# Optimization experiments

Measured on AMD Instinct MI355X. Metric: run time of the kernel, lower is better.

Reference implementation:

```python
import jax, jax.numpy as jnp
import numpy as np

H = 1024
V_IN = 32000
V_OUT = 32000
MAX_LEN = 512
SOS = 0


def _gru_cell(x, h, W_ih, W_hh, b_ih, b_hh):
    # PyTorch GRU cell: gates ordered (r, z, n)
    gi = W_ih @ x + b_ih            # [3H]
    gh = W_hh @ h + b_hh            # [3H]
    i_r, i_z, i_n = jnp.split(gi, 3)
    h_r, h_z, h_n = jnp.split(gh, 3)
    r = jax.nn.sigmoid(i_r + h_r)
    z = jax.nn.sigmoid(i_z + h_z)
    n = jnp.tanh(i_n + r * h_n)
    return (1.0 - z) * n + z * h


def setup_inputs() -> dict:
    key = jax.random.key(0)
    ks = jax.random.split(key, 20)
    s = 0.02
    f = jnp.float32
    d = {}
    d["input_tensor"] = jax.random.randint(ks[0], (512,), 0, V_IN)
    d["target_tensor"] = jax.random.randint(ks[1], (512,), 0, V_OUT)
    d["enc_emb"] = jax.random.normal(ks[2], (V_IN, H), f) * s
    d["enc_W_ih"] = jax.random.normal(ks[3], (3 * H, H), f) * s
    d["enc_W_hh"] = jax.random.normal(ks[4], (3 * H, H), f) * s
    d["enc_b_ih"] = jnp.zeros((3 * H,), f)
    d["enc_b_hh"] = jnp.zeros((3 * H,), f)
    d["dec_emb"] = jax.random.normal(ks[5], (V_OUT, H), f) * s
    d["attn_W"] = jax.random.normal(ks[6], (MAX_LEN, 2 * H), f) * s
    d["attn_b"] = jnp.zeros((MAX_LEN,), f)
    d["comb_W"] = jax.random.normal(ks[7], (H, 2 * H), f) * s
    d["comb_b"] = jnp.zeros((H,), f)
    d["dec_W_ih"] = jax.random.normal(ks[8], (3 * H, H), f) * s
    d["dec_W_hh"] = jax.random.normal(ks[9], (3 * H, H), f) * s
    d["dec_b_ih"] = jnp.zeros((3 * H,), f)
    d["dec_b_hh"] = jnp.zeros((3 * H,), f)
    d["out_W"] = jax.random.normal(ks[10], (V_OUT, H), f) * s
    d["out_b"] = jnp.zeros((V_OUT,), f)
    return d


def reference(input_tensor, target_tensor, enc_emb, enc_W_ih, enc_W_hh,
              enc_b_ih, enc_b_hh, dec_emb, attn_W, attn_b, comb_W, comb_b,
              dec_W_ih, dec_W_hh, dec_b_ih, dec_b_hh, out_W, out_b):
    # --- encoder: per-token GRU ---
    def enc_step(h, tok):
        x = enc_emb[tok]
        h2 = _gru_cell(x, h, enc_W_ih, enc_W_hh, enc_b_ih, enc_b_hh)
        return h2, h2

    h0 = jnp.zeros((H,), enc_emb.dtype)
    h_final, enc_outs = jax.lax.scan(enc_step, h0, input_tensor)
    # zero-padded encoder memory of size max_length (as in original)
    enc_full = jnp.zeros((MAX_LEN, H), enc_outs.dtype).at[: enc_outs.shape[0]].set(enc_outs)

    # --- decoder (teacher forcing): inputs are [SOS, target[:-1]] ---
    dec_in = jnp.concatenate([jnp.array([SOS], dtype=target_tensor.dtype),
                              target_tensor[:-1]])

    def dec_step(h, inp):
        tok, tgt = inp
        e = dec_emb[tok]                                        # [H]
        aw = jax.nn.softmax(attn_W @ jnp.concatenate([e, h]) + attn_b)  # [MAX_LEN]
        applied = aw @ enc_full                                 # [H]
        x = jax.nn.relu(comb_W @ jnp.concatenate([e, applied]) + comb_b)
        h2 = _gru_cell(x, h, dec_W_ih, dec_W_hh, dec_b_ih, dec_b_hh)
        logp = jax.nn.log_softmax(out_W @ h2 + out_b)           # [V_OUT]
        return h2, -logp[tgt]

    _, nll = jax.lax.scan(dec_step, h_final, (dec_in, target_tensor))
    return jnp.sum(nll) / target_tensor.shape[0]
```

## Files before the change

### kernel.cpp

```cpp
#include <hip/hip_runtime.h>
#include <math.h>


#define H 1024
#define T 512
#define V 32000

typedef unsigned long long u64;

__device__ __forceinline__ void st_agent_f32(float* p, float v) {
    __hip_atomic_store(p, v, __ATOMIC_RELAXED, __HIP_MEMORY_SCOPE_AGENT);
}
__device__ __forceinline__ float2 ld_agent_f2(const float* p) {
    u64 u = __hip_atomic_load((const u64*)p, __ATOMIC_RELAXED,
                              __HIP_MEMORY_SCOPE_AGENT);
    float2 t;
    __builtin_memcpy(&t, &u, 8);
    return t;
}
__device__ __forceinline__ void st_slot(unsigned* p, unsigned v) {
    __hip_atomic_store(p, v, __ATOMIC_RELAXED, __HIP_MEMORY_SCOPE_AGENT);
}
__device__ __forceinline__ unsigned ld_slot(const unsigned* p) {
    return __hip_atomic_load(p, __ATOMIC_RELAXED, __HIP_MEMORY_SCOPE_AGENT);
}

__device__ __forceinline__ void poll_slots(const unsigned* slots, unsigned val,
                                           int lane) {
    for (;;) {
        unsigned a = ld_slot(slots + (lane      ) * 16);
        unsigned b = ld_slot(slots + (lane +  64) * 16);
        unsigned c = ld_slot(slots + (lane + 128) * 16);
        unsigned d = ld_slot(slots + (lane + 192) * 16);
        int ok = (a >= val) & (b >= val) & (c >= val) & (d >= val);
        if (__all(ok)) break;
    }
}

__device__ __forceinline__ float sigmoidf_(float x) { return 1.f / (1.f + expf(-x)); }

__global__ __launch_bounds__(256) void gemm_tn(
    const float* __restrict__ X, int xs, int xo,
    const int* __restrict__ gidx, int gmode,
    const float* __restrict__ W, int wsd, int wo,
    const float* __restrict__ bias,
    float* __restrict__ C, int cs, int K)
{
    __shared__ float A_lds[32][64];
    __shared__ float B_lds[32][64];
    const int tid = threadIdx.x;
    const int tx = tid & 15, ty = tid >> 4;
    const int n0 = blockIdx.x * 64, t0 = blockIdx.y * 64;
    float acc[4][4] = {};

    for (int k0 = 0; k0 < K; k0 += 32) {
        #pragma unroll
        for (int q = 0; q < 2; ++q) {
            int f4 = tid + q * 256;
            int row = f4 >> 3, c4 = f4 & 7;
            int trow = t0 + row;
            const float* xr;
            if (gmode == 0)      xr = X + (size_t)trow * xs + xo;
            else if (gmode == 1) xr = X + (size_t)gidx[trow] * xs + xo;
            else { int tok = (trow == 0) ? 0 : gidx[trow - 1];
                   xr = X + (size_t)tok * xs + xo; }
            float4 a = *(const float4*)(xr + k0 + c4 * 4);
            A_lds[c4*4+0][row] = a.x; A_lds[c4*4+1][row] = a.y;
            A_lds[c4*4+2][row] = a.z; A_lds[c4*4+3][row] = a.w;
            const float* wr = W + (size_t)(n0 + row) * wsd + wo;
            float4 b = *(const float4*)(wr + k0 + c4 * 4);
            B_lds[c4*4+0][row] = b.x; B_lds[c4*4+1][row] = b.y;
            B_lds[c4*4+2][row] = b.z; B_lds[c4*4+3][row] = b.w;
        }
        __syncthreads();
        #pragma unroll
        for (int kk = 0; kk < 32; ++kk) {
            float4 a = *(const float4*)&A_lds[kk][ty * 4];
            float4 b = *(const float4*)&B_lds[kk][tx * 4];
            float av[4] = {a.x, a.y, a.z, a.w};
            float bv[4] = {b.x, b.y, b.z, b.w};
            #pragma unroll
            for (int i = 0; i < 4; ++i)
                #pragma unroll
                for (int j = 0; j < 4; ++j)
                    acc[i][j] = fmaf(av[i], bv[j], acc[i][j]);
        }
        __syncthreads();
    }
    float bj[4];
    #pragma unroll
    for (int j = 0; j < 4; ++j) bj[j] = bias ? bias[n0 + tx * 4 + j] : 0.f;
    #pragma unroll
    for (int i = 0; i < 4; ++i)
        #pragma unroll
        for (int j = 0; j < 4; ++j)
            C[(size_t)(t0 + ty * 4 + i) * cs + n0 + tx * 4 + j] = acc[i][j] + bj[j];
}

__global__ __launch_bounds__(512) void enc_seq(
    const float* __restrict__ Whh, const float* __restrict__ bhh,
    const float* __restrict__ gi,
    float* __restrict__ enc_outs,
    unsigned* __restrict__ slots)
{
    __shared__ float4 w4[12 * 256];
    __shared__ float h_lds[1024];
    __shared__ float gh_lds[12];
    __shared__ float bias_lds[12];
    const int tid = threadIdx.x, bid = blockIdx.x;
    const int j0 = bid * 4;
    for (int i = tid; i < 12 * 256; i += 512) {
        int r = i >> 8, c = i & 255;
        int grow = (r >> 2) * 1024 + j0 + (r & 3);
        w4[i] = *(const float4*)(Whh + (size_t)grow * 1024 + c * 4);
    }
    if (tid < 12) bias_lds[tid] = bhh[(tid >> 2) * 1024 + j0 + (tid & 3)];
    __syncthreads();

    const int wid = tid >> 6, lane = tid & 63;
    for (int t = 0; t < T; ++t) {
        if (t == 0) {
            if (tid < 256) ((float4*)h_lds)[tid] = make_float4(0.f, 0.f, 0.f, 0.f);
        } else {
            ((float2*)h_lds)[tid] =
                ld_agent_f2(enc_outs + (size_t)(t - 1) * 1024 + tid * 2);
        }
        float gir = 0.f, giz = 0.f, gin = 0.f;
        if (tid < 4) {
            const float* gr = gi + (size_t)t * 3072 + j0 + tid;
            gir = gr[0]; giz = gr[1024]; gin = gr[2048];
        }
        __syncthreads();
        for (int rr = wid; rr < 12; rr += 8) {
            const float4* wrow = w4 + rr * 256;
            float acc = 0.f;
            #pragma unroll
            for (int i = 0; i < 4; ++i) {
                float4 wv = wrow[lane + 64 * i];
                float4 hv = ((const float4*)h_lds)[lane + 64 * i];
                acc += wv.x*hv.x + wv.y*hv.y + wv.z*hv.z + wv.w*hv.w;
            }
            #pragma unroll
            for (int o = 32; o; o >>= 1) acc += __shfl_xor(acc, o);
            if (lane == 0) gh_lds[rr] = acc + bias_lds[rr];
        }
        __syncthreads();
        if (tid < 4) {
            float r = sigmoidf_(gir + gh_lds[tid]);
            float z = sigmoidf_(giz + gh_lds[4 + tid]);
            float n = tanhf(gin + r * gh_lds[8 + tid]);
            float hp = h_lds[j0 + tid];
            st_agent_f32(enc_outs + (size_t)t * 1024 + j0 + tid,
                         (1.f - z) * n + z * hp);
        }
        if (t < T - 1) {
            if (wid == 0) {
                asm volatile("s_waitcnt vmcnt(0)" ::: "memory");
                if (lane == 0) st_slot(slots + bid * 16, (unsigned)(t + 1));
                poll_slots(slots, (unsigned)(t + 1), lane);
            }
            __syncthreads();
        }
    }
}

__global__ __launch_bounds__(512) void dec_seq(
    const float* __restrict__ Wih, const float* __restrict__ Whh,
    const float* __restrict__ bih, const float* __restrict__ bhh,
    const float* __restrict__ attnW,
    const float* __restrict__ attn_e,
    const float* __restrict__ comb_e,
    const float* __restrict__ M,
    const float* __restrict__ enc_outs,
    float* __restrict__ H2,
    float* __restrict__ s_buf, float* __restrict__ x_buf,
    unsigned* __restrict__ slots)
{
    __shared__ float4 wih4[12 * 256];
    __shared__ float4 whh4[12 * 256];
    __shared__ float4 aw4[2 * 256];
    __shared__ float4 m4[4 * 128];
    __shared__ float h_lds[1024];
    __shared__ float x_lds[1024];
    __shared__ float p_lds[512];
    __shared__ float gh_lds[12], gi_lds[12];
    __shared__ float bih_lds[12], bhh_lds[12];

    const int tid = threadIdx.x, bid = blockIdx.x;
    const int j0 = bid * 4, l0 = bid * 2;
    for (int i = tid; i < 12 * 256; i += 512) {
        int r = i >> 8, c = i & 255;
        int grow = (r >> 2) * 1024 + j0 + (r & 3);
        wih4[i] = *(const float4*)(Wih + (size_t)grow * 1024 + c * 4);
        whh4[i] = *(const float4*)(Whh + (size_t)grow * 1024 + c * 4);
    }
    for (int i = tid; i < 2 * 256; i += 512) {
        int r = i >> 8, c = i & 255;
        aw4[i] = *(const float4*)(attnW + (size_t)(l0 + r) * 2048 + 1024 + c * 4);
    }
    for (int i = tid; i < 4 * 128; i += 512) {
        int r = i >> 7, c = i & 127;
        m4[i] = *(const float4*)(M + (size_t)(j0 + r) * 512 + c * 4);
    }
    if (tid < 12) {
        int grow = (tid >> 2) * 1024 + j0 + (tid & 3);
        bih_lds[tid] = bih[grow]; bhh_lds[tid] = bhh[grow];
    }
    __syncthreads();

    const int wid = tid >> 6, lane = tid & 63;
    for (int t = 0; t < T; ++t) {
        const float* hsrc = (t == 0) ? (enc_outs + (size_t)(T - 1) * 1024)
                                     : (H2 + (size_t)(t - 1) * 1024);
        ((float2*)h_lds)[tid] = ld_agent_f2(hsrc + tid * 2);
        float ae = 0.f, ce = 0.f;
        if (wid == 0 && (lane & 31) == 0)
            ae = attn_e[(size_t)t * 512 + l0 + (lane >> 5)];
        if (wid == 0 && (lane & 15) == 0)
            ce = comb_e[(size_t)t * 1024 + j0 + (lane >> 4)];
        __syncthreads();

        if (wid == 0) {
            {
                int r = lane >> 5, q2 = lane & 31;
                const float4* arow = aw4 + r * 256;
                float acc = 0.f;
                #pragma unroll
                for (int i = 0; i < 8; ++i) {
                    float4 wv = arow[q2 + 32 * i];
                    float4 hv = ((const float4*)h_lds)[q2 + 32 * i];
                    acc += wv.x*hv.x + wv.y*hv.y + wv.z*hv.z + wv.w*hv.w;
                }
                #pragma unroll
                for (int o = 16; o; o >>= 1) acc += __shfl_xor(acc, o);
                if (q2 == 0) st_agent_f32(s_buf + l0 + r, acc + ae);
            }
            asm volatile("s_waitcnt vmcnt(0)" ::: "memory");
            if (lane == 0) st_slot(slots + bid * 16, (unsigned)(3 * t + 1));
            poll_slots(slots, (unsigned)(3 * t + 1), lane);

            float sv[8];
            {
                float2 v0 = ld_agent_f2(s_buf + lane * 8);
                float2 v1 = ld_agent_f2(s_buf + lane * 8 + 2);
                float2 v2 = ld_agent_f2(s_buf + lane * 8 + 4);
                float2 v3 = ld_agent_f2(s_buf + lane * 8 + 6);
                sv[0]=v0.x; sv[1]=v0.y; sv[2]=v1.x; sv[3]=v1.y;
                sv[4]=v2.x; sv[5]=v2.y; sv[6]=v3.x; sv[7]=v3.y;
            }
            float mx = sv[0];
            #pragma unroll
            for (int j = 1; j < 8; ++j) mx = fmaxf(mx, sv[j]);
            #pragma unroll
            for (int o = 32; o; o >>= 1) mx = fmaxf(mx, __shfl_xor(mx, o));
            float pv[8], ssum = 0.f;
            #pragma unroll
            for (int j = 0; j < 8; ++j) { pv[j] = expf(sv[j] - mx); ssum += pv[j]; }
            #pragma unroll
            for (int o = 32; o; o >>= 1) ssum += __shfl_xor(ssum, o);
            ((float4*)p_lds)[lane * 2]     = make_float4(pv[0], pv[1], pv[2], pv[3]);
            ((float4*)p_lds)[lane * 2 + 1] = make_float4(pv[4], pv[5], pv[6], pv[7]);
            asm volatile("s_waitcnt lgkmcnt(0)" ::: "memory");
            {
                int d = lane >> 4, q = lane & 15;
                const float4* mr = m4 + d * 128;
                float acc = 0.f;
                #pragma unroll
                for (int i = 0; i < 8; ++i) {
                    float4 mv = mr[q + 16 * i];
                    float4 pp = ((const float4*)p_lds)[q + 16 * i];
                    acc += mv.x*pp.x + mv.y*pp.y + mv.z*pp.z + mv.w*pp.w;
                }
                #pragma unroll
                for (int o = 8; o; o >>= 1) acc += __shfl_xor(acc, o);
                if (q == 0)
                    st_agent_f32(x_buf + j0 + d, fmaxf(ce + acc / ssum, 0.f));
            }
            asm volatile("s_waitcnt vmcnt(0)" ::: "memory");
            if (lane == 0) st_slot(slots + bid * 16, (unsigned)(3 * t + 2));
            poll_slots(slots, (unsigned)(3 * t + 2), lane);
        } else {
            for (int rr = wid - 1; rr < 12; rr += 7) {
                const float4* wrow = whh4 + rr * 256;
                float acc = 0.f;
                #pragma unroll
                for (int i = 0; i < 4; ++i) {
                    float4 wv = wrow[lane + 64 * i];
                    float4 hv = ((const float4*)h_lds)[lane + 64 * i];
                    acc += wv.x*hv.x + wv.y*hv.y + wv.z*hv.z + wv.w*hv.w;
                }
                #pragma unroll
                for (int o = 32; o; o >>= 1) acc += __shfl_xor(acc, o);
                if (lane == 0) gh_lds[rr] = acc + bhh_lds[rr];
            }
        }
        __syncthreads();

        ((float2*)x_lds)[tid] = ld_agent_f2(x_buf + tid * 2);
        __syncthreads();
        for (int rr = wid; rr < 12; rr += 8) {
            const float4* wrow = wih4 + rr * 256;
            float acc = 0.f;
            #pragma unroll
            for (int i = 0; i < 4; ++i) {
                float4 wv = wrow[lane + 64 * i];
                float4 xv = ((const float4*)x_lds)[lane + 64 * i];
                acc += wv.x*xv.x + wv.y*xv.y + wv.z*xv.z + wv.w*xv.w;
            }
            #pragma unroll
            for (int o = 32; o; o >>= 1) acc += __shfl_xor(acc, o);
            if (lane == 0) gi_lds[rr] = acc + bih_lds[rr];
        }
        __syncthreads();
        if (tid < 4) {
            float r = sigmoidf_(gi_lds[tid] + gh_lds[tid]);
            float z = sigmoidf_(gi_lds[4 + tid] + gh_lds[4 + tid]);
            float n = tanhf(gi_lds[8 + tid] + r * gh_lds[8 + tid]);
            float hp = h_lds[j0 + tid];
            st_agent_f32(H2 + (size_t)t * 1024 + j0 + tid,
                         (1.f - z) * n + z * hp);
        }
        if (t < T - 1) {
            if (wid == 0) {
                asm volatile("s_waitcnt vmcnt(0)" ::: "memory");
                if (lane == 0) st_slot(slots + bid * 16, (unsigned)(3 * t + 3));
                poll_slots(slots, (unsigned)(3 * t + 3), lane);
            }
            __syncthreads();
        }
    }
}

__global__ __launch_bounds__(256) void out_gemm_lse(
    const float* __restrict__ H2, const float* __restrict__ outW,
    const float* __restrict__ outB, const int* __restrict__ tgt,
    float* __restrict__ lsep, float* __restrict__ tgtlog)
{
    __shared__ float A_lds[32][128];
    __shared__ float B_lds[32][128];
    const int tid = threadIdx.x;
    const int tx = tid & 15, ty = tid >> 4;
    const int c0 = blockIdx.x * 128, r0 = blockIdx.y * 128;
    float acc[8][8] = {};

    for (int k0 = 0; k0 < 1024; k0 += 32) {
        #pragma unroll
        for (int q = 0; q < 4; ++q) {
            int f4 = tid + q * 256;
            int row = f4 >> 3, c4 = f4 & 7;
            float4 a = *(const float4*)(H2 + (size_t)(r0 + row) * 1024 + k0 + c4 * 4);
            A_lds[c4*4+0][row] = a.x; A_lds[c4*4+1][row] = a.y;
            A_lds[c4*4+2][row] = a.z; A_lds[c4*4+3][row] = a.w;
            float4 b = *(const float4*)(outW + (size_t)(c0 + row) * 1024 + k0 + c4 * 4);
            B_lds[c4*4+0][row] = b.x; B_lds[c4*4+1][row] = b.y;
            B_lds[c4*4+2][row] = b.z; B_lds[c4*4+3][row] = b.w;
        }
        __syncthreads();
        #pragma unroll
        for (int kk = 0; kk < 32; ++kk) {
            float4 a0 = *(const float4*)&A_lds[kk][ty * 8];
            float4 a1 = *(const float4*)&A_lds[kk][ty * 8 + 4];
            float4 b0 = *(const float4*)&B_lds[kk][tx * 8];
            float4 b1 = *(const float4*)&B_lds[kk][tx * 8 + 4];
            float av[8] = {a0.x,a0.y,a0.z,a0.w,a1.x,a1.y,a1.z,a1.w};
            float bv[8] = {b0.x,b0.y,b0.z,b0.w,b1.x,b1.y,b1.z,b1.w};
            #pragma unroll
            for (int i = 0; i < 8; ++i)
                #pragma unroll
                for (int j = 0; j < 8; ++j)
                    acc[i][j] = fmaf(av[i], bv[j], acc[i][j]);
        }
        __syncthreads();
    }
    float bj[8];
    #pragma unroll
    for (int j = 0; j < 8; ++j) bj[j] = outB[c0 + tx * 8 + j];

    const int bx = blockIdx.x;
    #pragma unroll
    for (int i = 0; i < 8; ++i) {
        int t = r0 + ty * 8 + i;
// ... 45 lines not shown
    if ((t & 63) == 0) red[t >> 6] = v;
    __syncthreads();
    if (t == 0) {
        float sum = 0.f;
        for (int w = 0; w < 8; ++w) sum += red[w];
        out[0] = sum / 512.f;
    }
}

extern "C" void kernel_launch(void* const* d_in, const int* in_sizes, int n_in,
                              void* d_out, int out_size, void* d_ws, size_t ws_size,
                              hipStream_t stream) {
    const int*   input   = (const int*)d_in[0];
    const int*   target  = (const int*)d_in[1];
    const float* enc_emb = (const float*)d_in[2];
    const float* eWih    = (const float*)d_in[3];
    const float* eWhh    = (const float*)d_in[4];
    const float* ebih    = (const float*)d_in[5];
    const float* ebhh    = (const float*)d_in[6];
    const float* dec_emb = (const float*)d_in[7];
    const float* attnW   = (const float*)d_in[8];
    const float* attnB   = (const float*)d_in[9];
    const float* combW   = (const float*)d_in[10];
    const float* combB   = (const float*)d_in[11];
    const float* dWih    = (const float*)d_in[12];
    const float* dWhh    = (const float*)d_in[13];
    const float* dbih    = (const float*)d_in[14];
    const float* dbhh    = (const float*)d_in[15];
    const float* outW    = (const float*)d_in[16];
    const float* outB    = (const float*)d_in[17];
    float* out = (float*)d_out;

    float* wsf = (float*)d_ws;
    unsigned* slotsE = (unsigned*)d_ws;
    unsigned* slotsD = (unsigned*)((char*)d_ws + 16384);
    float* enc_gi   = wsf + 8192;
    float* enc_outs = wsf + 1581056;
    float* attn_e   = wsf + 2105344;
    float* comb_e   = wsf + 2367488;
    float* Mws      = wsf + 2891776;
    float* H2       = wsf + 3416064;
    float* s_buf    = wsf + 3940352;
    float* x_buf    = wsf + 3940864;
    float* lsep     = wsf + 3941888;
    float* tgtlog   = wsf + 4197888;

    hipMemsetAsync(d_ws, 0, 32768, stream);

    gemm_tn<<<dim3(48, 8), 256, 0, stream>>>(enc_emb, 1024, 0, input, 1,
        eWih, 1024, 0, ebih, enc_gi, 3072, 1024);
    gemm_tn<<<dim3(8, 8), 256, 0, stream>>>(dec_emb, 1024, 0, target, 2,
        attnW, 2048, 0, attnB, attn_e, 512, 1024);
    gemm_tn<<<dim3(16, 8), 256, 0, stream>>>(dec_emb, 1024, 0, target, 2,
        combW, 2048, 0, combB, comb_e, 1024, 1024);

    enc_seq<<<256, 512, 0, stream>>>(eWhh, ebhh, enc_gi, enc_outs, slotsE);

    gemm_tn<<<dim3(8, 16), 256, 0, stream>>>(combW, 2048, 1024, nullptr, 0,
        enc_outs, 1024, 0, nullptr, Mws, 512, 1024);

    dec_seq<<<256, 512, 0, stream>>>(dWih, dWhh, dbih, dbhh, attnW,
        attn_e, comb_e, Mws, enc_outs, H2, s_buf, x_buf, slotsD);

    out_gemm_lse<<<dim3(250, 4), 256, 0, stream>>>(H2, outW, outB, target,
        lsep, tgtlog);

    lse_combine<<<1, 512, 0, stream>>>(lsep, tgtlog, out);
}
```

Baseline: 7.380 ms.

## Replace slot barriers with tagged LL flag-data exchange and single-wave blocks

Replaces the global counter-slot barriers in the encoder and decoder persistent kernels with LL-style 64-bit stores that pack a step tag with each value. Consumers poll the data buffers directly, so a separate flag write and reload after each barrier is no longer needed. Blocks shrink from 512 threads to one 64-lane wave, which serializes the per-block matvec rows onto that single wave but removes intra-block syncs and the wait on the memory counter. The aim is lower per-step grid synchronization latency on the recurrent critical path, at the cost of less parallel compute per block.

```diff
diff --git a/kernel.cpp b/kernel.cpp
--- a/kernel.cpp
+++ b/kernel.cpp
@@ -8,33 +8,41 @@
 
 typedef unsigned long long u64;
 
-__device__ __forceinline__ void st_agent_f32(float* p, float v) {
-    __hip_atomic_store(p, v, __ATOMIC_RELAXED, __HIP_MEMORY_SCOPE_AGENT);
-}
-__device__ __forceinline__ float2 ld_agent_f2(const float* p) {
-    u64 u = __hip_atomic_load((const u64*)p, __ATOMIC_RELAXED,
-                              __HIP_MEMORY_SCOPE_AGENT);
-    float2 t;
-    __builtin_memcpy(&t, &u, 8);
-    return t;
-}
-__device__ __forceinline__ void st_slot(unsigned* p, unsigned v) {
-    __hip_atomic_store(p, v, __ATOMIC_RELAXED, __HIP_MEMORY_SCOPE_AGENT);
-}
-__device__ __forceinline__ unsigned ld_slot(const unsigned* p) {
-    return __hip_atomic_load(p, __ATOMIC_RELAXED, __HIP_MEMORY_SCOPE_AGENT);
-}
-
-__device__ __forceinline__ void poll_slots(const unsigned* slots, unsigned val,
-                                           int lane) {
+__device__ __forceinline__ void ll_store(u64* seg, float v, unsigned tag) {
+    u64 p = ((u64)tag << 32) | (u64)__float_as_uint(v);
+    __hip_atomic_store(seg, p, __ATOMIC_RELAXED, __HIP_MEMORY_SCOPE_AGENT);
+}
+__device__ __forceinline__ void ll_poll8(const u64* buf, unsigned tag, int lane,
+                                         float* out) {
+    u64 v[8];
     for (;;) {
-        unsigned a = ld_slot(slots + (lane      ) * 16);
-        unsigned b = ld_slot(slots + (lane +  64) * 16);
-        unsigned c = ld_slot(slots + (lane + 128) * 16);
-        unsigned d = ld_slot(slots + (lane + 192) * 16);
-        int ok = (a >= val) & (b >= val) & (c >= val) & (d >= val);
+        #pragma unroll
+        for (int j = 0; j < 8; ++j)
+            v[j] = __hip_atomic_load(buf + lane + 64 * j, __ATOMIC_RELAXED,
+                                     __HIP_MEMORY_SCOPE_AGENT);
+        int ok = 1;
+        #pragma unroll
+        for (int j = 0; j < 8; ++j) ok &= ((unsigned)(v[j] >> 32) >= tag);
         if (__all(ok)) break;
     }
+    #pragma unroll
+    for (int j = 0; j < 8; ++j) out[j] = __uint_as_float((unsigned)v[j]);
+}
+__device__ __forceinline__ void ll_poll16(const u64* buf, unsigned tag, int lane,
+                                          float* out) {
+    u64 v[16];
+    for (;;) {
+        #pragma unroll
+        for (int j = 0; j < 16; ++j)
+            v[j] = __hip_atomic_load(buf + lane + 64 * j, __ATOMIC_RELAXED,
+                                     __HIP_MEMORY_SCOPE_AGENT);
+        int ok = 1;
+        #pragma unroll
+        for (int j = 0; j < 16; ++j) ok &= ((unsigned)(v[j] >> 32) >= tag);
+        if (__all(ok)) break;
+    }
+    #pragma unroll
+    for (int j = 0; j < 16; ++j) out[j] = __uint_as_float((unsigned)v[j]);
 }
 
 __device__ __forceinline__ float sigmoidf_(float x) { return 1.f / (1.f + expf(-x)); }
@@ -97,41 +105,35 @@
             C[(size_t)(t0 + ty * 4 + i) * cs + n0 + tx * 4 + j] = acc[i][j] + bj[j];
 }
 
-__global__ __launch_bounds__(512) void enc_seq(
+__global__ __launch_bounds__(64) void enc_seq(
     const float* __restrict__ Whh, const float* __restrict__ bhh,
     const float* __restrict__ gi,
     float* __restrict__ enc_outs,
-    unsigned* __restrict__ slots)
+    u64* __restrict__ hb)
 {
     __shared__ float4 w4[12 * 256];
     __shared__ float h_lds[1024];
     __shared__ float gh_lds[12];
     __shared__ float bias_lds[12];
-    const int tid = threadIdx.x, bid = blockIdx.x;
+    const int lane = threadIdx.x, bid = blockIdx.x;
     const int j0 = bid * 4;
-    for (int i = tid; i < 12 * 256; i += 512) {
+    for (int i = lane; i < 12 * 256; i += 64) {
         int r = i >> 8, c = i & 255;
         int grow = (r >> 2) * 1024 + j0 + (r & 3);
         w4[i] = *(const float4*)(Whh + (size_t)grow * 1024 + c * 4);
     }
-    if (tid < 12) bias_lds[tid] = bhh[(tid >> 2) * 1024 + j0 + (tid & 3)];
+    if (lane < 12) bias_lds[lane] = bhh[(lane >> 2) * 1024 + j0 + (lane & 3)];
+    #pragma unroll
+    for (int j = 0; j < 16; ++j) h_lds[lane + 64 * j] = 0.f;
     __syncthreads();
 
-    const int wid = tid >> 6, lane = tid & 63;
     for (int t = 0; t < T; ++t) {
-        if (t == 0) {
-            if (tid < 256) ((float4*)h_lds)[tid] = make_float4(0.f, 0.f, 0.f, 0.f);
-        } else {
-            ((float2*)h_lds)[tid] =
-                ld_agent_f2(enc_outs + (size_t)(t - 1) * 1024 + tid * 2);
-        }
         float gir = 0.f, giz = 0.f, gin = 0.f;
-        if (tid < 4) {
-            const float* gr = gi + (size_t)t * 3072 + j0 + tid;
+        if (lane < 4) {
+            const float* gr = gi + (size_t)t * 3072 + j0 + lane;
             gir = gr[0]; giz = gr[1024]; gin = gr[2048];
         }
-        __syncthreads();
-        for (int rr = wid; rr < 12; rr += 8) {
+        for (int rr = 0; rr < 12; ++rr) {
             const float4* wrow = w4 + rr * 256;
             float acc = 0.f;
             #pragma unroll
@@ -145,26 +147,25 @@
             if (lane == 0) gh_lds[rr] = acc + bias_lds[rr];
         }
         __syncthreads();
-        if (tid < 4) {
-            float r = sigmoidf_(gir + gh_lds[tid]);
-            float z = sigmoidf_(giz + gh_lds[4 + tid]);
-            float n = tanhf(gin + r * gh_lds[8 + tid]);
-            float hp = h_lds[j0 + tid];
-            st_agent_f32(enc_outs + (size_t)t * 1024 + j0 + tid,
-                         (1.f - z) * n + z * hp);
+        if (lane < 4) {
+            float r = sigmoidf_(gir + gh_lds[lane]);
+            float z = sigmoidf_(giz + gh_lds[4 + lane]);
+            float n = tanhf(gin + r * gh_lds[8 + lane]);
+            float h2 = (1.f - z) * n + z * h_lds[j0 + lane];
+            enc_outs[(size_t)t * 1024 + j0 + lane] = h2;
+            ll_store(hb + (t & 1) * 1024 + j0 + lane, h2, (unsigned)(t + 1));
         }
         if (t < T - 1) {
-            if (wid == 0) {
-                asm volatile("s_waitcnt vmcnt(0)" ::: "memory");
-                if (lane == 0) st_slot(slots + bid * 16, (unsigned)(t + 1));
-                poll_slots(slots, (unsigned)(t + 1), lane);
-            }
+            float hv[16];
+            ll_poll16(hb + (t & 1) * 1024, (unsigned)(t + 1), lane, hv);
+            #pragma unroll
+            for (int j = 0; j < 16; ++j) h_lds[lane + 64 * j] = hv[j];
             __syncthreads();
         }
     }
 }
 
-__global__ __launch_bounds__(512) void dec_seq(
+__global__ __launch_bounds__(64) void dec_seq(
     const float* __restrict__ Wih, const float* __restrict__ Whh,
     const float* __restrict__ bih, const float* __restrict__ bhh,
     const float* __restrict__ attnW,
@@ -173,8 +174,7 @@
     const float* __restrict__ M,
     const float* __restrict__ enc_outs,
     float* __restrict__ H2,
-    float* __restrict__ s_buf, float* __restrict__ x_buf,
-    unsigned* __restrict__ slots)
+    u64* __restrict__ sb, u64* __restrict__ xb, u64* __restrict__ hb)
 {
     __shared__ float4 wih4[12 * 256];
     __shared__ float4 whh4[12 * 256];
@@ -186,146 +186,131 @@
     __shared__ float gh_lds[12], gi_lds[12];
     __shared__ float bih_lds[12], bhh_lds[12];
 
-    const int tid = threadIdx.x, bid = blockIdx.x;
+    const int lane = threadIdx.x, bid = blockIdx.x;
     const int j0 = bid * 4, l0 = bid * 2;
-    for (int i = tid; i < 12 * 256; i += 512) {
+    for (int i = lane; i < 12 * 256; i += 64) {
         int r = i >> 8, c = i & 255;
         int grow = (r >> 2) * 1024 + j0 + (r & 3);
         wih4[i] = *(const float4*)(Wih + (size_t)grow * 1024 + c * 4);
         whh4[i] = *(const float4*)(Whh + (size_t)grow * 1024 + c * 4);
     }
-    for (int i = tid; i < 2 * 256; i += 512) {
+    for (int i = lane; i < 2 * 256; i += 64) {
         int r = i >> 8, c = i & 255;
         aw4[i] = *(const float4*)(attnW + (size_t)(l0 + r) * 2048 + 1024 + c * 4);
     }
-    for (int i = tid; i < 4 * 128; i += 512) {
+    for (int i = lane; i < 4 * 128; i += 64) {
         int r = i >> 7, c = i & 127;
         m4[i] = *(const float4*)(M + (size_t)(j0 + r) * 512 + c * 4);
     }
-    if (tid < 12) {
-        int grow = (tid >> 2) * 1024 + j0 + (tid & 3);
-        bih_lds[tid] = bih[grow]; bhh_lds[tid] = bhh[grow];
-    }
+    if (lane < 12) {
+        int grow = (lane >> 2) * 1024 + j0 + (lane & 3);
+        bih_lds[lane] = bih[grow]; bhh_lds[lane] = bhh[grow];
+    }
+    #pragma unroll
+    for (int j = 0; j < 16; ++j)
+        h_lds[lane + 64 * j] = enc_outs[(size_t)(T - 1) * 1024 + lane + 64 * j];
     __syncthreads();
 
-    const int wid = tid >> 6, lane = tid & 63;
     for (int t = 0; t < T; ++t) {
-        const float* hsrc = (t == 0) ? (enc_outs + (size_t)(T - 1) * 1024)
-                                     : (H2 + (size_t)(t - 1) * 1024);
-        ((float2*)h_lds)[tid] = ld_agent_f2(hsrc + tid * 2);
+        const unsigned tag = (unsigned)(t + 1);
         float ae = 0.f, ce = 0.f;
-        if (wid == 0 && (lane & 31) == 0)
-            ae = attn_e[(size_t)t * 512 + l0 + (lane >> 5)];
-        if (wid == 0 && (lane & 15) == 0)
-            ce = comb_e[(size_t)t * 1024 + j0 + (lane >> 4)];
-        __syncthreads();
-
-        if (wid == 0) {
-            {
-                int r = lane >> 5, q2 = lane & 31;
-                const float4* arow = aw4 + r * 256;
-                float acc = 0.f;
-                #pragma unroll
-                for (int i = 0; i < 8; ++i) {
-                    float4 wv = arow[q2 + 32 * i];
-                    float4 hv = ((const float4*)h_lds)[q2 + 32 * i];
-                    acc += wv.x*hv.x + wv.y*hv.y + wv.z*hv.z + wv.w*hv.w;
-                }
-                #pragma unroll
-                for (int o = 16; o; o >>= 1) acc += __shfl_xor(acc, o);
-                if (q2 == 0) st_agent_f32(s_buf + l0 + r, acc + ae);
+        if ((lane & 31) == 0) ae = attn_e[(size_t)t * 512 + l0 + (lane >> 5)];
+        if ((lane & 15) == 0) ce = comb_e[(size_t)t * 1024 + j0 + (lane >> 4)];
+
+        {
+            const float4* arow = aw4 + (lane >> 5) * 256;
+            const int q2 = lane & 31;
+            float acc = 0.f;
+            #pragma unroll
+            for (int i = 0; i < 8; ++i) {
+                float4 wv = arow[q2 + 32 * i];
+                float4 hv = ((const float4*)h_lds)[q2 + 32 * i];
+                acc += wv.x*hv.x + wv.y*hv.y + wv.z*hv.z + wv.w*hv.w;
             }
-            asm volatile("s_waitcnt vmcnt(0)" ::: "memory");
-            if (lane == 0) st_slot(slots + bid * 16, (unsigned)(3 * t + 1));
-            poll_slots(slots, (unsigned)(3 * t + 1), lane);
-
-            float sv[8];
-            {
-                float2 v0 = ld_agent_f2(s_buf + lane * 8);
-                float2 v1 = ld_agent_f2(s_buf + lane * 8 + 2);
-                float2 v2 = ld_agent_f2(s_buf + lane * 8 + 4);
-                float2 v3 = ld_agent_f2(s_buf + lane * 8 + 6);
-                sv[0]=v0.x; sv[1]=v0.y; sv[2]=v1.x; sv[3]=v1.y;
-                sv[4]=v2.x; sv[5]=v2.y; sv[6]=v3.x; sv[7]=v3.y;
+            #pragma unroll
+            for (int o = 16; o; o >>= 1) acc += __shfl_xor(acc, o);
+            if (q2 == 0) ll_store(sb + l0 + (lane >> 5), acc + ae, tag);
+        }
+
+        for (int rr = 0; rr < 12; ++rr) {
+            const float4* wrow = whh4 + rr * 256;
+            float acc = 0.f;
+            #pragma unroll
+            for (int i = 0; i < 4; ++i) {
+                float4 wv = wrow[lane + 64 * i];
+                float4 hv = ((const float4*)h_lds)[lane + 64 * i];
+                acc += wv.x*hv.x + wv.y*hv.y + wv.z*hv.z + wv.w*hv.w;
             }
-            float mx = sv[0];
-            #pragma unroll
-            for (int j = 1; j < 8; ++j) mx = fmaxf(mx, sv[j]);
-            #pragma unroll
-            for (int o = 32; o; o >>= 1) mx = fmaxf(mx, __shfl_xor(mx, o));
-            float pv[8], ssum = 0.f;
-            #pragma unroll
-            for (int j = 0; j < 8; ++j) { pv[j] = expf(sv[j] - mx); ssum += pv[j]; }
-            #pragma unroll
-            for (int o = 32; o; o >>= 1) ssum += __shfl_xor(ssum, o);
-            ((float4*)p_lds)[lane * 2]     = make_float4(pv[0], pv[1], pv[2], pv[3]);
-            ((float4*)p_lds)[lane * 2 + 1] = make_float4(pv[4], pv[5], pv[6], pv[7]);
-            asm volatile("s_waitcnt lgkmcnt(0)" ::: "memory");
-            {
-                int d = lane >> 4, q = lane & 15;
-                const float4* mr = m4 + d * 128;
-                float acc = 0.f;
-                #pragma unroll
-                for (int i = 0; i < 8; ++i) {
-                    float4 mv = mr[q + 16 * i];
-                    float4 pp = ((const float4*)p_lds)[q + 16 * i];
-                    acc += mv.x*pp.x + mv.y*pp.y + mv.z*pp.z + mv.w*pp.w;
-                }
-                #pragma unroll
-                for (int o = 8; o; o >>= 1) acc += __shfl_xor(acc, o);
-                if (q == 0)
-                    st_agent_f32(x_buf + j0 + d, fmaxf(ce + acc / ssum, 0.f));
+            #pragma unroll
+            for (int o = 32; o; o >>= 1) acc += __shfl_xor(acc, o);
+            if (lane == 0) gh_lds[rr] = acc + bhh_lds[rr];
+        }
+
+        float sv[8];
+        ll_poll8(sb, tag, lane, sv);
+        float mx = sv[0];
+        #pragma unroll
+        for (int j = 1; j < 8; ++j) mx = fmaxf(mx, sv[j]);
+        #pragma unroll
+        for (int o = 32; o; o >>= 1) mx = fmaxf(mx, __shfl_xor(mx, o));
+        float pv[8], lsum = 0.f;
+        #pragma unroll
+        for (int j = 0; j < 8; ++j) { pv[j] = expf(sv[j] - mx); lsum += pv[j]; }
+        #pragma unroll
+        for (int o = 32; o; o >>= 1) lsum += __shfl_xor(lsum, o);
+        #pragma unroll
+        for (int j = 0; j < 8; ++j) p_lds[lane + 64 * j] = pv[j];
+        __syncthreads();
+
+        {
+            const int d = lane >> 4, q = lane & 15;
+            const float4* mr = m4 + d * 128;
+            float acc = 0.f;
+            #pragma unroll
+            for (int i = 0; i < 8; ++i) {
+                float4 mv = mr[q + 16 * i];
+                float4 pp = ((const float4*)p_lds)[q + 16 * i];
+                acc += mv.x*pp.x + mv.y*pp.y + mv.z*pp.z + mv.w*pp.w;
             }
-            asm volatile("s_waitcnt vmcnt(0)" ::: "memory");
-            if (lane == 0) st_slot(slots + bid * 16, (unsigned)(3 * t + 2));
-            poll_slots(slots, (unsigned)(3 * t + 2), lane);
-        } else {
-            for (int rr = wid - 1; rr < 12; rr += 7) {
-                const float4* wrow = whh4 + rr * 256;
-                float acc = 0.f;
-                #pragma unroll
-                for (int i = 0; i < 4; ++i) {
-                    float4 wv = wrow[lane + 64 * i];
-                    float4 hv = ((const float4*)h_lds)[lane + 64 * i];
-                    acc += wv.x*hv.x + wv.y*hv.y + wv.z*hv.z + wv.w*hv.w;
-                }
-                #pragma unroll
-                for (int o = 32; o; o >>= 1) acc += __shfl_xor(acc, o);
-                if (lane == 0) gh_lds[rr] = acc + bhh_lds[rr];
-            }
-        }
-        __syncthreads();
-
-        ((float2*)x_lds)[tid] = ld_agent_f2(x_buf + tid * 2);
-        __syncthreads();
-        for (int rr = wid; rr < 12; rr += 8) {
+            #pragma unroll
+            for (int o = 8; o; o >>= 1) acc += __shfl_xor(acc, o);
+            if (q == 0)
+                ll_store(xb + j0 + d, fmaxf(ce + acc / lsum, 0.f), tag);
+        }
+
+        float xv[16];
+        ll_poll16(xb, tag, lane, xv);
+        #pragma unroll
+        for (int j = 0; j < 16; ++j) x_lds[lane + 64 * j] = xv[j];
+        __syncthreads();
+        for (int rr = 0; rr < 12; ++rr) {
             const float4* wrow = wih4 + rr * 256;
             float acc = 0.f;
             #pragma unroll
             for (int i = 0; i < 4; ++i) {
                 float4 wv = wrow[lane + 64 * i];
-                float4 xv = ((const float4*)x_lds)[lane + 64 * i];
-                acc += wv.x*xv.x + wv.y*xv.y + wv.z*xv.z + wv.w*xv.w;
+                float4 xvv = ((const float4*)x_lds)[lane + 64 * i];
+                acc += wv.x*xvv.x + wv.y*xvv.y + wv.z*xvv.z + wv.w*xvv.w;
             }
             #pragma unroll
             for (int o = 32; o; o >>= 1) acc += __shfl_xor(acc, o);
             if (lane == 0) gi_lds[rr] = acc + bih_lds[rr];
         }
         __syncthreads();
-        if (tid < 4) {
-            float r = sigmoidf_(gi_lds[tid] + gh_lds[tid]);
-            float z = sigmoidf_(gi_lds[4 + tid] + gh_lds[4 + tid]);
-            float n = tanhf(gi_lds[8 + tid] + r * gh_lds[8 + tid]);
-            float hp = h_lds[j0 + tid];
-            st_agent_f32(H2 + (size_t)t * 1024 + j0 + tid,
-                         (1.f - z) * n + z * hp);
+
+        if (lane < 4) {
+            float r = sigmoidf_(gi_lds[lane] + gh_lds[lane]);
+            float z = sigmoidf_(gi_lds[4 + lane] + gh_lds[4 + lane]);
+            float n = tanhf(gi_lds[8 + lane] + r * gh_lds[8 + lane]);
+            float h2 = (1.f - z) * n + z * h_lds[j0 + lane];
+            H2[(size_t)t * 1024 + j0 + lane] = h2;
+            ll_store(hb + j0 + lane, h2, tag);
         }
         if (t < T - 1) {
-            if (wid == 0) {
-                asm volatile("s_waitcnt vmcnt(0)" ::: "memory");
-                if (lane == 0) st_slot(slots + bid * 16, (unsigned)(3 * t + 3));
-                poll_slots(slots, (unsigned)(3 * t + 3), lane);
-            }
+            float hv[16];
+            ll_poll16(hb, tag, lane, hv);
+            #pragma unroll
+            for (int j = 0; j < 16; ++j) h_lds[lane + 64 * j] = hv[j];
             __syncthreads();
         }
     }
@@ -458,20 +443,20 @@
     float* out = (float*)d_out;
 
     float* wsf = (float*)d_ws;
-    unsigned* slotsE = (unsigned*)d_ws;
-    unsigned* slotsD = (unsigned*)((char*)d_ws + 16384);
-    float* enc_gi   = wsf + 8192;
-    float* enc_outs = wsf + 1581056;
-    float* attn_e   = wsf + 2105344;
-    float* comb_e   = wsf + 2367488;
-    float* Mws      = wsf + 2891776;
-    float* H2       = wsf + 3416064;
-    float* s_buf    = wsf + 3940352;
-    float* x_buf    = wsf + 3940864;
-    float* lsep     = wsf + 3941888;
-    float* tgtlog   = wsf + 4197888;
-
-    hipMemsetAsync(d_ws, 0, 32768, stream);
+    u64* encHB = (u64*)d_ws;
+    u64* SB    = (u64*)((char*)d_ws + 16384);
+    u64* XB    = (u64*)((char*)d_ws + 20480);
+    u64* HB    = (u64*)((char*)d_ws + 28672);
+    float* enc_gi   = wsf + 9216;
+    float* enc_outs = wsf + 1582080;
+    float* attn_e   = wsf + 2106368;
+    float* comb_e   = wsf + 2368512;
+    float* Mws      = wsf + 2892800;
+    float* H2       = wsf + 3417088;
+    float* lsep     = wsf + 3941376;
+    float* tgtlog   = wsf + 4197376;
+
+    hipMemsetAsync(d_ws, 0, 36864, stream);
 
     gemm_tn<<<dim3(48, 8), 256, 0, stream>>>(enc_emb, 1024, 0, input, 1,
         eWih, 1024, 0, ebih, enc_gi, 3072, 1024);
@@ -480,13 +465,13 @@
     gemm_tn<<<dim3(16, 8), 256, 0, stream>>>(dec_emb, 1024, 0, target, 2,
         combW, 2048, 0, combB, comb_e, 1024, 1024);
 
-    enc_seq<<<256, 512, 0, stream>>>(eWhh, ebhh, enc_gi, enc_outs, slotsE);
+    enc_seq<<<256, 64, 0, stream>>>(eWhh, ebhh, enc_gi, enc_outs, encHB);
 
     gemm_tn<<<dim3(8, 16), 256, 0, stream>>>(combW, 2048, 1024, nullptr, 0,
         enc_outs, 1024, 0, nullptr, Mws, 512, 1024);
 
-    dec_seq<<<256, 512, 0, stream>>>(dWih, dWhh, dbih, dbhh, attnW,
-        attn_e, comb_e, Mws, enc_outs, H2, s_buf, x_buf, slotsD);
+    dec_seq<<<256, 64, 0, stream>>>(dWih, dWhh, dbih, dbhh, attnW,
+        attn_e, comb_e, Mws, enc_outs, H2, SB, XB, HB);
 
     out_gemm_lse<<<dim3(250, 4), 256, 0, stream>>>(H2, outW, outB, target,
         lsep, tgtlog);
```

New measurement: 9.939 ms. 1.35x slower.

## Shrink persistent RNN blocks to 256 threads with packed per-phase flag arrays

Applied to the files above, without the earlier changes.

The persistent encoder and decoder kernels now run with 256 threads per block. Each 16-lane group computes one gate row, instead of each 64-lane wave striding over rows. The grid barrier moves from padded per-block slots with one monotonically increasing counter to contiguous flag arrays, one per decoder phase. After the barrier, wave 0 alone reloads the new hidden state into LDS, removing a block-wide sync per step. The aim is to cut the latency of cross-block synchronisation and barriers on the serial critical path. Packing the flags into adjacent words risks more cache-line contention while blocks poll.

```diff
diff --git a/kernel.cpp b/kernel.cpp
--- a/kernel.cpp
+++ b/kernel.cpp
@@ -10,6 +10,12 @@
 
 __device__ __forceinline__ void st_agent_f32(float* p, float v) {
     __hip_atomic_store(p, v, __ATOMIC_RELAXED, __HIP_MEMORY_SCOPE_AGENT);
+}
+__device__ __forceinline__ void st_agent_u32(unsigned* p, unsigned v) {
+    __hip_atomic_store(p, v, __ATOMIC_RELAXED, __HIP_MEMORY_SCOPE_AGENT);
+}
+__device__ __forceinline__ unsigned ld_agent_u32(const unsigned* p) {
+    return __hip_atomic_load(p, __ATOMIC_RELAXED, __HIP_MEMORY_SCOPE_AGENT);
 }
 __device__ __forceinline__ float2 ld_agent_f2(const float* p) {
     u64 u = __hip_atomic_load((const u64*)p, __ATOMIC_RELAXED,
@@ -18,24 +24,18 @@
     __builtin_memcpy(&t, &u, 8);
     return t;
 }
-__device__ __forceinline__ void st_slot(unsigned* p, unsigned v) {
-    __hip_atomic_store(p, v, __ATOMIC_RELAXED, __HIP_MEMORY_SCOPE_AGENT);
-}
-__device__ __forceinline__ unsigned ld_slot(const unsigned* p) {
-    return __hip_atomic_load(p, __ATOMIC_RELAXED, __HIP_MEMORY_SCOPE_AGENT);
-}
-
-__device__ __forceinline__ void poll_slots(const unsigned* slots, unsigned val,
+__device__ __forceinline__ void poll_flags(const unsigned* f, unsigned tag,
                                            int lane) {
     for (;;) {
-        unsigned a = ld_slot(slots + (lane      ) * 16);
-        unsigned b = ld_slot(slots + (lane +  64) * 16);
-        unsigned c = ld_slot(slots + (lane + 128) * 16);
-        unsigned d = ld_slot(slots + (lane + 192) * 16);
-        int ok = (a >= val) & (b >= val) & (c >= val) & (d >= val);
+        unsigned a = ld_agent_u32(f + lane);
+        unsigned b = ld_agent_u32(f + lane + 64);
+        unsigned c = ld_agent_u32(f + lane + 128);
+        unsigned d = ld_agent_u32(f + lane + 192);
+        int ok = (a >= tag) & (b >= tag) & (c >= tag) & (d >= tag);
         if (__all(ok)) break;
     }
 }
+#define VMCNT0() asm volatile("s_waitcnt vmcnt(0)" ::: "memory")
 
 __device__ __forceinline__ float sigmoidf_(float x) { return 1.f / (1.f + expf(-x)); }
 
@@ -55,8 +55,8 @@
 
     for (int k0 = 0; k0 < K; k0 += 32) {
         #pragma unroll
-        for (int q = 0; q < 2; ++q) {
-            int f4 = tid + q * 256;
+        for (int qq = 0; qq < 2; ++qq) {
+            int f4 = tid + qq * 256;
             int row = f4 >> 3, c4 = f4 & 7;
             int trow = t0 + row;
             const float* xr;
@@ -97,74 +97,74 @@
             C[(size_t)(t0 + ty * 4 + i) * cs + n0 + tx * 4 + j] = acc[i][j] + bj[j];
 }
 
-__global__ __launch_bounds__(512) void enc_seq(
+__global__ __launch_bounds__(256) void enc_seq(
     const float* __restrict__ Whh, const float* __restrict__ bhh,
     const float* __restrict__ gi,
     float* __restrict__ enc_outs,
-    unsigned* __restrict__ slots)
+    unsigned* __restrict__ flags)
 {
     __shared__ float4 w4[12 * 256];
     __shared__ float h_lds[1024];
     __shared__ float gh_lds[12];
     __shared__ float bias_lds[12];
     const int tid = threadIdx.x, bid = blockIdx.x;
+    const int wid = tid >> 6, lane = tid & 63;
+    const int g = tid >> 4, q = tid & 15;
     const int j0 = bid * 4;
-    for (int i = tid; i < 12 * 256; i += 512) {
+
+    for (int i = tid; i < 12 * 256; i += 256) {
         int r = i >> 8, c = i & 255;
         int grow = (r >> 2) * 1024 + j0 + (r & 3);
         w4[i] = *(const float4*)(Whh + (size_t)grow * 1024 + c * 4);
     }
     if (tid < 12) bias_lds[tid] = bhh[(tid >> 2) * 1024 + j0 + (tid & 3)];
+    ((float4*)h_lds)[tid] = make_float4(0.f, 0.f, 0.f, 0.f);
     __syncthreads();
 
-    const int wid = tid >> 6, lane = tid & 63;
     for (int t = 0; t < T; ++t) {
-        if (t == 0) {
-            if (tid < 256) ((float4*)h_lds)[tid] = make_float4(0.f, 0.f, 0.f, 0.f);
-        } else {
-            ((float2*)h_lds)[tid] =
-                ld_agent_f2(enc_outs + (size_t)(t - 1) * 1024 + tid * 2);
-        }
         float gir = 0.f, giz = 0.f, gin = 0.f;
-        if (tid < 4) {
-            const float* gr = gi + (size_t)t * 3072 + j0 + tid;
+        if (wid == 0 && lane < 4) {
+            const float* gr = gi + (size_t)t * 3072 + j0 + lane;
             gir = gr[0]; giz = gr[1024]; gin = gr[2048];
         }
-        __syncthreads();
-        for (int rr = wid; rr < 12; rr += 8) {
-            const float4* wrow = w4 + rr * 256;
+        if (g < 12) {
+            const float4* wrow = w4 + g * 256;
             float acc = 0.f;
             #pragma unroll
-            for (int i = 0; i < 4; ++i) {
-                float4 wv = wrow[lane + 64 * i];
-                float4 hv = ((const float4*)h_lds)[lane + 64 * i];
+            for (int i = 0; i < 16; ++i) {
+                float4 wv = wrow[q + 16 * i];
+                float4 hv = ((const float4*)h_lds)[q + 16 * i];
                 acc += wv.x*hv.x + wv.y*hv.y + wv.z*hv.z + wv.w*hv.w;
             }
             #pragma unroll
-            for (int o = 32; o; o >>= 1) acc += __shfl_xor(acc, o);
-            if (lane == 0) gh_lds[rr] = acc + bias_lds[rr];
-        }
-        __syncthreads();
-        if (tid < 4) {
-            float r = sigmoidf_(gir + gh_lds[tid]);
-            float z = sigmoidf_(giz + gh_lds[4 + tid]);
-            float n = tanhf(gin + r * gh_lds[8 + tid]);
-            float hp = h_lds[j0 + tid];
-            st_agent_f32(enc_outs + (size_t)t * 1024 + j0 + tid,
-                         (1.f - z) * n + z * hp);
-        }
-        if (t < T - 1) {
-            if (wid == 0) {
-                asm volatile("s_waitcnt vmcnt(0)" ::: "memory");
-                if (lane == 0) st_slot(slots + bid * 16, (unsigned)(t + 1));
-                poll_slots(slots, (unsigned)(t + 1), lane);
-            }
-            __syncthreads();
-        }
-    }
-}
-
-__global__ __launch_bounds__(512) void dec_seq(
+            for (int o = 8; o; o >>= 1) acc += __shfl_xor(acc, o);
+            if (q == 0) gh_lds[g] = acc + bias_lds[g];
+        }
+        __syncthreads();
+        if (wid == 0) {
+            if (lane < 4) {
+                float r = sigmoidf_(gir + gh_lds[lane]);
+                float z = sigmoidf_(giz + gh_lds[4 + lane]);
+                float n = tanhf(gin + r * gh_lds[8 + lane]);
+                st_agent_f32(enc_outs + (size_t)t * 1024 + j0 + lane,
+                             (1.f - z) * n + z * h_lds[j0 + lane]);
+            }
+            if (t < T - 1) {
+                VMCNT0();
+                if (lane == 0) st_agent_u32(flags + bid, (unsigned)(t + 1));
+                poll_flags(flags, (unsigned)(t + 1), lane);
+                const float* hr = enc_outs + (size_t)t * 1024;
+                #pragma unroll
+                for (int k = 0; k < 8; ++k)
+                    ((float2*)h_lds)[lane + 64 * k] =
+                        ld_agent_f2(hr + lane * 2 + 128 * k);
+            }
+        }
+        if (t < T - 1) __syncthreads();
+    }
+}
+
+__global__ __launch_bounds__(256) void dec_seq(
     const float* __restrict__ Wih, const float* __restrict__ Whh,
     const float* __restrict__ bih, const float* __restrict__ bhh,
     const float* __restrict__ attnW,
@@ -174,7 +174,8 @@
     const float* __restrict__ enc_outs,
     float* __restrict__ H2,
     float* __restrict__ s_buf, float* __restrict__ x_buf,
-    unsigned* __restrict__ slots)
+    unsigned* __restrict__ sF, unsigned* __restrict__ xF,
+    unsigned* __restrict__ hF)
 {
     __shared__ float4 wih4[12 * 256];
     __shared__ float4 whh4[12 * 256];
@@ -187,18 +188,21 @@
     __shared__ float bih_lds[12], bhh_lds[12];
 
     const int tid = threadIdx.x, bid = blockIdx.x;
+    const int wid = tid >> 6, lane = tid & 63;
+    const int g = tid >> 4, q = tid & 15;
     const int j0 = bid * 4, l0 = bid * 2;
-    for (int i = tid; i < 12 * 256; i += 512) {
+
+    for (int i = tid; i < 12 * 256; i += 256) {
         int r = i >> 8, c = i & 255;
         int grow = (r >> 2) * 1024 + j0 + (r & 3);
         wih4[i] = *(const float4*)(Wih + (size_t)grow * 1024 + c * 4);
         whh4[i] = *(const float4*)(Whh + (size_t)grow * 1024 + c * 4);
     }
-    for (int i = tid; i < 2 * 256; i += 512) {
+    for (int i = tid; i < 2 * 256; i += 256) {
         int r = i >> 8, c = i & 255;
         aw4[i] = *(const float4*)(attnW + (size_t)(l0 + r) * 2048 + 1024 + c * 4);
     }
-    for (int i = tid; i < 4 * 128; i += 512) {
+    for (int i = tid; i < 4 * 128; i += 256) {
         int r = i >> 7, c = i & 127;
         m4[i] = *(const float4*)(M + (size_t)(j0 + r) * 512 + c * 4);
     }
@@ -206,24 +210,18 @@
         int grow = (tid >> 2) * 1024 + j0 + (tid & 3);
         bih_lds[tid] = bih[grow]; bhh_lds[tid] = bhh[grow];
     }
+    ((float4*)h_lds)[tid] = ((const float4*)(enc_outs + (size_t)(T - 1) * 1024))[tid];
     __syncthreads();
 
-    const int wid = tid >> 6, lane = tid & 63;
     for (int t = 0; t < T; ++t) {
-        const float* hsrc = (t == 0) ? (enc_outs + (size_t)(T - 1) * 1024)
-                                     : (H2 + (size_t)(t - 1) * 1024);
-        ((float2*)h_lds)[tid] = ld_agent_f2(hsrc + tid * 2);
-        float ae = 0.f, ce = 0.f;
-        if (wid == 0 && (lane & 31) == 0)
-            ae = attn_e[(size_t)t * 512 + l0 + (lane >> 5)];
-        if (wid == 0 && (lane & 15) == 0)
-            ce = comb_e[(size_t)t * 1024 + j0 + (lane >> 4)];
-        __syncthreads();
-
+        const unsigned tag = (unsigned)(t + 1);
         if (wid == 0) {
+            float ae = 0.f, ce = 0.f;
+            if ((lane & 31) == 0) ae = attn_e[(size_t)t * 512 + l0 + (lane >> 5)];
+            if ((lane & 15) == 0) ce = comb_e[(size_t)t * 1024 + j0 + (lane >> 4)];
             {
-                int r = lane >> 5, q2 = lane & 31;
-                const float4* arow = aw4 + r * 256;
+                const float4* arow = aw4 + (lane >> 5) * 256;
+                const int q2 = lane & 31;
                 float acc = 0.f;
                 #pragma unroll
                 for (int i = 0; i < 8; ++i) {
@@ -233,101 +231,101 @@
                 }
                 #pragma unroll
                 for (int o = 16; o; o >>= 1) acc += __shfl_xor(acc, o);
-                if (q2 == 0) st_agent_f32(s_buf + l0 + r, acc + ae);
-            }
-            asm volatile("s_waitcnt vmcnt(0)" ::: "memory");
-            if (lane == 0) st_slot(slots + bid * 16, (unsigned)(3 * t + 1));
-            poll_slots(slots, (unsigned)(3 * t + 1), lane);
-
+                if (q2 == 0) st_agent_f32(s_buf + l0 + (lane >> 5), acc + ae);
+            }
+            VMCNT0();
+            if (lane == 0) st_agent_u32(sF + bid, tag);
+            poll_flags(sF, tag, lane);
             float sv[8];
+            #pragma unroll
+            for (int k = 0; k < 4; ++k) {
+                float2 v = ld_agent_f2(s_buf + lane * 2 + 128 * k);
+                sv[2*k] = v.x; sv[2*k+1] = v.y;
+            }
+            float mx = sv[0];
+            #pragma unroll
+            for (int j = 1; j < 8; ++j) mx = fmaxf(mx, sv[j]);
+            #pragma unroll
+            for (int o = 32; o; o >>= 1) mx = fmaxf(mx, __shfl_xor(mx, o));
+            float ls = 0.f, pv[8];
+            #pragma unroll
+            for (int j = 0; j < 8; ++j) { pv[j] = expf(sv[j] - mx); ls += pv[j]; }
+            #pragma unroll
+            for (int o = 32; o; o >>= 1) ls += __shfl_xor(ls, o);
+            #pragma unroll
+            for (int k = 0; k < 4; ++k)
+                ((float2*)p_lds)[lane + 64 * k] = make_float2(pv[2*k], pv[2*k+1]);
             {
-                float2 v0 = ld_agent_f2(s_buf + lane * 8);
-                float2 v1 = ld_agent_f2(s_buf + lane * 8 + 2);
-                float2 v2 = ld_agent_f2(s_buf + lane * 8 + 4);
-                float2 v3 = ld_agent_f2(s_buf + lane * 8 + 6);
-                sv[0]=v0.x; sv[1]=v0.y; sv[2]=v1.x; sv[3]=v1.y;
-                sv[4]=v2.x; sv[5]=v2.y; sv[6]=v3.x; sv[7]=v3.y;
-            }
-            float mx = sv[0];
-            #pragma unroll
-            for (int j = 1; j < 8; ++j) mx = fmaxf(mx, sv[j]);
-            #pragma unroll
-            for (int o = 32; o; o >>= 1) mx = fmaxf(mx, __shfl_xor(mx, o));
-            float pv[8], ssum = 0.f;
-            #pragma unroll
-            for (int j = 0; j < 8; ++j) { pv[j] = expf(sv[j] - mx); ssum += pv[j]; }
-            #pragma unroll
-            for (int o = 32; o; o >>= 1) ssum += __shfl_xor(ssum, o);
-            ((float4*)p_lds)[lane * 2]     = make_float4(pv[0], pv[1], pv[2], pv[3]);
-            ((float4*)p_lds)[lane * 2 + 1] = make_float4(pv[4], pv[5], pv[6], pv[7]);
-            asm volatile("s_waitcnt lgkmcnt(0)" ::: "memory");
-            {
-                int d = lane >> 4, q = lane & 15;
+                const int d = lane >> 4, qq = lane & 15;
                 const float4* mr = m4 + d * 128;
                 float acc = 0.f;
                 #pragma unroll
                 for (int i = 0; i < 8; ++i) {
-                    float4 mv = mr[q + 16 * i];
-                    float4 pp = ((const float4*)p_lds)[q + 16 * i];
+                    float4 mv = mr[qq + 16 * i];
+                    float4 pp = ((const float4*)p_lds)[qq + 16 * i];
                     acc += mv.x*pp.x + mv.y*pp.y + mv.z*pp.z + mv.w*pp.w;
                 }
                 #pragma unroll
                 for (int o = 8; o; o >>= 1) acc += __shfl_xor(acc, o);
-                if (q == 0)
-                    st_agent_f32(x_buf + j0 + d, fmaxf(ce + acc / ssum, 0.f));
-            }
-            asm volatile("s_waitcnt vmcnt(0)" ::: "memory");
-            if (lane == 0) st_slot(slots + bid * 16, (unsigned)(3 * t + 2));
-            poll_slots(slots, (unsigned)(3 * t + 2), lane);
+                if (qq == 0)
+                    st_agent_f32(x_buf + j0 + d, fmaxf(ce + acc / ls, 0.f));
+            }
+            VMCNT0();
+            if (lane == 0) st_agent_u32(xF + bid, tag);
+            poll_flags(xF, tag, lane);
+            #pragma unroll
+            for (int k = 0; k < 8; ++k)
+                ((float2*)x_lds)[lane + 64 * k] =
+                    ld_agent_f2(x_buf + lane * 2 + 128 * k);
         } else {
-            for (int rr = wid - 1; rr < 12; rr += 7) {
-                const float4* wrow = whh4 + rr * 256;
-                float acc = 0.f;
-                #pragma unroll
-                for (int i = 0; i < 4; ++i) {
-                    float4 wv = wrow[lane + 64 * i];
-                    float4 hv = ((const float4*)h_lds)[lane + 64 * i];
-                    acc += wv.x*hv.x + wv.y*hv.y + wv.z*hv.z + wv.w*hv.w;
-                }
-                #pragma unroll
-                for (int o = 32; o; o >>= 1) acc += __shfl_xor(acc, o);
-                if (lane == 0) gh_lds[rr] = acc + bhh_lds[rr];
-            }
-        }
-        __syncthreads();
-
-        ((float2*)x_lds)[tid] = ld_agent_f2(x_buf + tid * 2);
-        __syncthreads();
-        for (int rr = wid; rr < 12; rr += 8) {
-            const float4* wrow = wih4 + rr * 256;
+            const int gg = g - 4;
+            const float4* wrow = whh4 + gg * 256;
             float acc = 0.f;
             #pragma unroll
-            for (int i = 0; i < 4; ++i) {
-                float4 wv = wrow[lane + 64 * i];
-                float4 xv = ((const float4*)x_lds)[lane + 64 * i];
+            for (int i = 0; i < 16; ++i) {
+                float4 wv = wrow[q + 16 * i];
+                float4 hv = ((const float4*)h_lds)[q + 16 * i];
+                acc += wv.x*hv.x + wv.y*hv.y + wv.z*hv.z + wv.w*hv.w;
+            }
+            #pragma unroll
+            for (int o = 8; o; o >>= 1) acc += __shfl_xor(acc, o);
+            if (q == 0) gh_lds[gg] = acc + bhh_lds[gg];
+        }
+        __syncthreads();
+        if (g < 12) {
+            const float4* wrow = wih4 + g * 256;
+            float acc = 0.f;
+            #pragma unroll
+            for (int i = 0; i < 16; ++i) {
+                float4 wv = wrow[q + 16 * i];
+                float4 xv = ((const float4*)x_lds)[q + 16 * i];
                 acc += wv.x*xv.x + wv.y*xv.y + wv.z*xv.z + wv.w*xv.w;
             }
             #pragma unroll
-            for (int o = 32; o; o >>= 1) acc += __shfl_xor(acc, o);
-            if (lane == 0) gi_lds[rr] = acc + bih_lds[rr];
-        }
-        __syncthreads();
-        if (tid < 4) {
-            float r = sigmoidf_(gi_lds[tid] + gh_lds[tid]);
-            float z = sigmoidf_(gi_lds[4 + tid] + gh_lds[4 + tid]);
-            float n = tanhf(gi_lds[8 + tid] + r * gh_lds[8 + tid]);
-            float hp = h_lds[j0 + tid];
-            st_agent_f32(H2 + (size_t)t * 1024 + j0 + tid,
-                         (1.f - z) * n + z * hp);
-        }
-        if (t < T - 1) {
-            if (wid == 0) {
-                asm volatile("s_waitcnt vmcnt(0)" ::: "memory");
-                if (lane == 0) st_slot(slots + bid * 16, (unsigned)(3 * t + 3));
-                poll_slots(slots, (unsigned)(3 * t + 3), lane);
-            }
-            __syncthreads();
-        }
+            for (int o = 8; o; o >>= 1) acc += __shfl_xor(acc, o);
+            if (q == 0) gi_lds[g] = acc + bih_lds[g];
+        }
+        __syncthreads();
+        if (wid == 0) {
+            if (lane < 4) {
+                float r = sigmoidf_(gi_lds[lane] + gh_lds[lane]);
+                float z = sigmoidf_(gi_lds[4 + lane] + gh_lds[4 + lane]);
+                float n = tanhf(gi_lds[8 + lane] + r * gh_lds[8 + lane]);
+                st_agent_f32(H2 + (size_t)t * 1024 + j0 + lane,
+                             (1.f - z) * n + z * h_lds[j0 + lane]);
+            }
+            if (t < T - 1) {
+                VMCNT0();
+                if (lane == 0) st_agent_u32(hF + bid, tag);
+                poll_flags(hF, tag, lane);
+                const float* hr = H2 + (size_t)t * 1024;
+                #pragma unroll
+                for (int k = 0; k < 8; ++k)
+                    ((float2*)h_lds)[lane + 64 * k] =
+                        ld_agent_f2(hr + lane * 2 + 128 * k);
+            }
+        }
+        if (t < T - 1) __syncthreads();
     }
 }
 
@@ -345,8 +343,8 @@
 
     for (int k0 = 0; k0 < 1024; k0 += 32) {
         #pragma unroll
-        for (int q = 0; q < 4; ++q) {
-            int f4 = tid + q * 256;
+        for (int qq = 0; qq < 4; ++qq) {
+            int f4 = tid + qq * 256;
             int row = f4 >> 3, c4 = f4 & 7;
             float4 a = *(const float4*)(H2 + (size_t)(r0 + row) * 1024 + k0 + c4 * 4);
             A_lds[c4*4+0][row] = a.x; A_lds[c4*4+1][row] = a.y;
@@ -458,20 +456,22 @@
     float* out = (float*)d_out;
 
     float* wsf = (float*)d_ws;
-    unsigned* slotsE = (unsigned*)d_ws;
-    unsigned* slotsD = (unsigned*)((char*)d_ws + 16384);
-    float* enc_gi   = wsf + 8192;
-    float* enc_outs = wsf + 1581056;
-    float* attn_e   = wsf + 2105344;
-    float* comb_e   = wsf + 2367488;
-    float* Mws      = wsf + 2891776;
-    float* H2       = wsf + 3416064;
-    float* s_buf    = wsf + 3940352;
-    float* x_buf    = wsf + 3940864;
-    float* lsep     = wsf + 3941888;
-    float* tgtlog   = wsf + 4197888;
-
-    hipMemsetAsync(d_ws, 0, 32768, stream);
+    unsigned* encF = (unsigned*)d_ws;
+    unsigned* sF   = (unsigned*)((char*)d_ws + 1024);
+    unsigned* xF   = (unsigned*)((char*)d_ws + 2048);
+    unsigned* hF   = (unsigned*)((char*)d_ws + 3072);
+    float* enc_gi   = wsf + 1024;
+    float* enc_outs = wsf + 1573888;
+    float* attn_e   = wsf + 2098176;
+    float* comb_e   = wsf + 2360320;
+    float* Mws      = wsf + 2884608;
+    float* H2       = wsf + 3408896;
+    float* s_buf    = wsf + 3933184;
+    float* x_buf    = wsf + 3933696;
+    float* lsep     = wsf + 3934720;
+    float* tgtlog   = wsf + 4190720;
+
+    hipMemsetAsync(d_ws, 0, 4096, stream);
 
     gemm_tn<<<dim3(48, 8), 256, 0, stream>>>(enc_emb, 1024, 0, input, 1,
         eWih, 1024, 0, ebih, enc_gi, 3072, 1024);
@@ -480,13 +480,13 @@
     gemm_tn<<<dim3(16, 8), 256, 0, stream>>>(dec_emb, 1024, 0, target, 2,
         combW, 2048, 0, combB, comb_e, 1024, 1024);
 
-    enc_seq<<<256, 512, 0, stream>>>(eWhh, ebhh, enc_gi, enc_outs, slotsE);
+    enc_seq<<<256, 256, 0, stream>>>(eWhh, ebhh, enc_gi, enc_outs, encF);
 
     gemm_tn<<<dim3(8, 16), 256, 0, stream>>>(combW, 2048, 1024, nullptr, 0,
         enc_outs, 1024, 0, nullptr, Mws, 512, 1024);
 
-    dec_seq<<<256, 512, 0, stream>>>(dWih, dWhh, dbih, dbhh, attnW,
-        attn_e, comb_e, Mws, enc_outs, H2, s_buf, x_buf, slotsD);
+    dec_seq<<<256, 256, 0, stream>>>(dWih, dWhh, dbih, dbhh, attnW,
+        attn_e, comb_e, Mws, enc_outs, H2, s_buf, x_buf, sF, xF, hF);
 
     out_gemm_lse<<<dim3(250, 4), 256, 0, stream>>>(H2, outW, outB, target,
         lsep, tgtlog);
```

Result: slower. 14.81 ms (+100.7%).
